# Kernel optimization log

Measured on AMD Instinct MI355X. Metric: run time of the kernel, lower is better.

The kernel has to match this reference:

```python
import jax, jax.numpy as jnp
import numpy as np

def setup_inputs() -> dict:
    key = jax.random.key(0)
    k1, k2, k3, k4 = jax.random.split(key, 4)
    B, T, C, D = 4, 4096, 1024, 128
    x = jax.random.normal(k1, (B, T, C), dtype=jnp.float32)
    Wq = jax.random.normal(k2, (C, D), dtype=jnp.float32) * (C ** -0.5)
    Wk = jax.random.normal(k3, (C, D), dtype=jnp.float32) * (C ** -0.5)
    Wv = jax.random.normal(k4, (C, D), dtype=jnp.float32) * (C ** -0.5)
    return {"x": x, "Wq": Wq, "Wk": Wk, "Wv": Wv}

def reference(x, Wq, Wk, Wv):
    # x: [B,T,C]; Wq/Wk/Wv: [C,D] (nn.Linear bias=False => x @ W)
    B, T, C = x.shape
    q = jnp.einsum('btc,cd->btd', x, Wq)  # [B,T,D]
    k = jnp.einsum('btc,cd->btd', x, Wk)
    v = jnp.einsum('btc,cd->btd', x, Wv)
    dk = q.shape[-1]
    scale = dk ** -0.5
    w = jnp.einsum('btd,bsd->bts', q, k) * scale  # [B,T,T]
    causal = jnp.tril(jnp.ones((T, T), dtype=bool))
    w = jnp.where(causal, w, -jnp.inf)
    w = jax.nn.softmax(w, axis=-1)
    # dropout p=0.0 => identity
    attention = jnp.einsum('bts,bsd->btd', w, v)  # [B,T,D]
    return attention
```

## Files before the change

kernel.cpp:

```cpp
#include <hip/hip_runtime.h>
#include <stdint.h>

typedef __bf16 bf16_t;
typedef bf16_t bf16x8 __attribute__((ext_vector_type(8)));
typedef float f32x4 __attribute__((ext_vector_type(4)));
typedef unsigned short us8 __attribute__((ext_vector_type(8)));
typedef unsigned short us4 __attribute__((ext_vector_type(4)));
typedef unsigned int u32x4 __attribute__((ext_vector_type(4)));

#define B_ 4
#define T_ 4096
#define C_ 1024
#define D_ 128

#define NCHUNK_PB 288
#define QSCALE 0.12751744f

__device__ __forceinline__ uint16_t f2bf(float f) {
    union { float f; uint32_t u; } v; v.f = f;
    uint32_t u = v.u;
    uint32_t r = (u + 0x7fffu + ((u >> 16) & 1u)) >> 16;
    return (uint16_t)r;
}

__device__ __forceinline__ uint16_t bfru(float f) {
    return (uint16_t)((__float_as_uint(f) + 0x8000u) >> 16);
}

__global__ __launch_bounds__(256) void prep_w(const float* __restrict__ Wq,
                                              const float* __restrict__ Wk,
                                              const float* __restrict__ Wv,
                                              uint16_t* __restrict__ WT) {
    int idx = blockIdx.x * 256 + threadIdx.x;
    if (idx >= 3 * D_ * C_) return;
    int w   = idx / (D_ * C_);
    int rem = idx - w * (D_ * C_);
    int n   = rem / C_;
    int k   = rem - n * C_;
    const float* W = (w == 0) ? Wq : (w == 1) ? Wk : Wv;
    WT[idx] = f2bf(W[(size_t)k * D_ + n]);
}

#define GST 72

__global__ __launch_bounds__(256) void qkv_gemm(const float* __restrict__ x,
                                                const uint16_t* __restrict__ WT,
                                                uint16_t* __restrict__ qb,
                                                uint16_t* __restrict__ kb,
                                                uint16_t* __restrict__ vT) {
    __shared__ __align__(16) uint16_t A_lds[64 * GST];
    __shared__ __align__(16) uint16_t W_lds[128 * GST];

    int tid  = threadIdx.x;
    int lane = tid & 63;
    int wave = tid >> 6;
    int quad = lane >> 4;
    int lx   = lane & 15;
    int wm   = wave >> 1, wn = wave & 1;

    int bx   = blockIdx.x;
    int wsel = bx % 3;
    int m0   = (bx / 3) * 64;
    const uint16_t* Wp = WT + (size_t)wsel * (D_ * C_);

    f32x4 acc[2][4];
    for (int mf = 0; mf < 2; mf++)
        for (int nf = 0; nf < 4; nf++)
            acc[mf][nf] = (f32x4){0.f, 0.f, 0.f, 0.f};

    int arow = tid >> 2, acb = (tid & 3) * 16;
    int wrow = tid >> 1, wcb = (tid & 1) * 32;

    for (int k0 = 0; k0 < C_; k0 += 64) {
        {
            const float* xp = x + (size_t)(m0 + arow) * C_ + k0 + acb;
            uint32_t d[8];
#pragma unroll
            for (int j = 0; j < 4; j++) {
                float4 f = *(const float4*)(xp + j * 4);
                uint32_t u0 = __float_as_uint(f.x) + 0x8000u;
                uint32_t u1 = __float_as_uint(f.y) + 0x8000u;
                uint32_t u2 = __float_as_uint(f.z) + 0x8000u;
                uint32_t u3 = __float_as_uint(f.w) + 0x8000u;
                d[2 * j]     = __builtin_amdgcn_perm(u1, u0, 0x07060302);
                d[2 * j + 1] = __builtin_amdgcn_perm(u3, u2, 0x07060302);
            }
            *(u32x4*)&A_lds[arow * GST + acb]     = (u32x4){d[0], d[1], d[2], d[3]};
            *(u32x4*)&A_lds[arow * GST + acb + 8] = (u32x4){d[4], d[5], d[6], d[7]};
        }
        {
            const uint16_t* wp = Wp + (size_t)wrow * C_ + k0 + wcb;
#pragma unroll
            for (int i = 0; i < 4; i++)
                *(us8*)&W_lds[wrow * GST + wcb + i * 8] = *(const us8*)(wp + i * 8);
        }
        __syncthreads();

#pragma unroll
        for (int kc = 0; kc < 2; kc++) {
            bf16x8 af[2];
#pragma unroll
            for (int mf = 0; mf < 2; mf++)
                af[mf] = *(const bf16x8*)&A_lds[(wm * 32 + mf * 16 + lx) * GST + kc * 32 + quad * 8];
#pragma unroll
            for (int nf = 0; nf < 4; nf++) {
                bf16x8 bf = *(const bf16x8*)&W_lds[(wn * 64 + nf * 16 + lx) * GST + kc * 32 + quad * 8];
                acc[0][nf] = __builtin_amdgcn_mfma_f32_16x16x32_bf16(af[0], bf, acc[0][nf], 0, 0, 0);
                acc[1][nf] = __builtin_amdgcn_mfma_f32_16x16x32_bf16(af[1], bf, acc[1][nf], 0, 0, 0);
            }
        }
        __syncthreads();
    }

    int mrow0 = m0 + wm * 32 + quad * 4;
    if (wsel == 2) {
#pragma unroll
        for (int mf = 0; mf < 2; mf++) {
            int mbase = mrow0 + mf * 16;
            int batch = mbase >> 12;
            int t     = mbase & 4095;
#pragma unroll
            for (int nf = 0; nf < 4; nf++) {
                int n = wn * 64 + nf * 16 + lx;
                us4 pv;
#pragma unroll
                for (int r = 0; r < 4; r++) pv[r] = bfru(acc[mf][nf][r]);
                *(us4*)&vT[(size_t)batch * D_ * T_ + (size_t)n * T_ + t] = pv;
            }
        }
    } else {
        uint16_t* dst = (wsel == 0) ? qb : kb;
        float sc = (wsel == 0) ? QSCALE : 1.0f;
#pragma unroll
        for (int mf = 0; mf < 2; mf++)
#pragma unroll
            for (int nf = 0; nf < 4; nf++) {
                int n = wn * 64 + nf * 16 + lx;
#pragma unroll
                for (int r = 0; r < 4; r++)
                    dst[(size_t)(mrow0 + mf * 16 + r) * D_ + n] = bfru(acc[mf][nf][r] * sc);
            }
    }
}

#define KST 136
#define VST 72

__global__ __launch_bounds__(256) void attn(const uint16_t* __restrict__ qb,
                                            const uint16_t* __restrict__ kb,
                                            const uint16_t* __restrict__ vT,
                                            float* __restrict__ part,
                                            float* __restrict__ ml) {
    __shared__ __align__(16) uint16_t K_lds[64 * KST];
    __shared__ __align__(16) uint16_t V_lds[144 * VST];
    __shared__ __align__(16) uint16_t P_lds[4][16 * VST];

    int tid  = threadIdx.x;
    int lane = tid & 63;
    int wave = tid >> 6;
    int quad = lane >> 4;
    int lx   = lane & 15;

    int batch = blockIdx.x & 3;
    int L     = NCHUNK_PB - 1 - (blockIdx.x >> 2);
    int g = 0;
    while (g < 7 && 4 * (g + 1) * (g + 2) <= L) g++;
    int rem   = L - 4 * g * (g + 1);
    int jt    = 8 * g + rem / (g + 1);
    int chunk = rem - (rem / (g + 1)) * (g + 1);
    int lidx  = batch * NCHUNK_PB + L;

    int q0     = jt * 64;
    int st0    = chunk * 8;
    int ntiles = min(8, jt - st0 + 1);

    for (int i = tid; i < 16 * VST; i += 256) {
        int r = i / VST;
        V_lds[(128 + r) * VST + (i - r * VST)] = (r == 0) ? 0x3F80 : 0;
    }

    bf16x8 qf[4];
    {
        const uint16_t* qp = qb + (size_t)(batch * T_ + q0 + wave * 16 + lx) * D_ + quad * 8;
#pragma unroll
        for (int kc = 0; kc < 4; kc++) qf[kc] = *(const bf16x8*)(qp + kc * 32);
    }

    f32x4 o[9];
    for (int i = 0; i < 9; i++) o[i] = (f32x4){0.f, 0.f, 0.f, 0.f};
    float m_i[4];
    for (int r = 0; r < 4; r++) m_i[r] = -INFINITY;

    int krow = tid >> 2, kcb = (tid & 3) * 32;
    int vd   = tid >> 1, vsb = (tid & 1) * 32;

    for (int it = 0; it < ntiles; it++) {
        int s0 = (st0 + it) * 64;
        {
            const uint16_t* kp = kb + (size_t)(batch * T_ + s0 + krow) * D_ + kcb;
#pragma unroll
            for (int i = 0; i < 4; i++)
                *(us8*)&K_lds[krow * KST + kcb + i * 8] = *(const us8*)(kp + i * 8);
        }
        {
            const uint16_t* vp = vT + (size_t)batch * D_ * T_ + (size_t)vd * T_ + s0 + vsb;
#pragma unroll
            for (int i = 0; i < 4; i++)
                *(us8*)&V_lds[vd * VST + vsb + i * 8] = *(const us8*)(vp + i * 8);
        }
        __syncthreads();

        f32x4 s[4];
        for (int nf = 0; nf < 4; nf++) s[nf] = (f32x4){0.f, 0.f, 0.f, 0.f};
#pragma unroll
        for (int kc = 0; kc < 4; kc++)
#pragma unroll
            for (int nf = 0; nf < 4; nf++) {
                bf16x8 kf = *(const bf16x8*)&K_lds[(nf * 16 + lx) * KST + kc * 32 + quad * 8];
                s[nf] = __builtin_amdgcn_mfma_f32_16x16x32_bf16(qf[kc], kf, s[nf], 0, 0, 0);
            }

        float p[4][4];
#pragma unroll
        for (int nf = 0; nf < 4; nf++)
#pragma unroll
            for (int r = 0; r < 4; r++) p[nf][r] = s[nf][r];

        if (st0 + it == jt) {
            int rowg = q0 + wave * 16 + quad * 4;
#pragma unroll
            for (int nf = 0; nf < 4; nf++) {
                int colg = s0 + nf * 16 + lx;
#pragma unroll
                for (int r = 0; r < 4; r++)
                    if (colg > rowg + r) p[nf][r] = -INFINITY;
            }
        }

        float rm[4];
#pragma unroll
        for (int r = 0; r < 4; r++)
            rm[r] = fmaxf(fmaxf(p[0][r], p[1][r]), fmaxf(p[2][r], p[3][r]));
#pragma unroll
        for (int off = 1; off < 16; off <<= 1)
#pragma unroll
            for (int r = 0; r < 4; r++)
                rm[r] = fmaxf(rm[r], __shfl_xor(rm[r], off, 64));

        float alpha[4];
#pragma unroll
        for (int r = 0; r < 4; r++) {
            float mn = fmaxf(m_i[r], rm[r]);
            alpha[r] = exp2f(m_i[r] - mn);
            m_i[r]   = mn;
#pragma unroll
            for (int nf = 0; nf < 4; nf++)
                p[nf][r] = exp2f(p[nf][r] - mn);
        }
#pragma unroll
        for (int i = 0; i < 9; i++)
#pragma unroll
            for (int r = 0; r < 4; r++) o[i][r] *= alpha[r];

#pragma unroll
        for (int nf = 0; nf < 4; nf++)
#pragma unroll
            for (int r = 0; r < 4; r++) {
                uint32_t u  = __float_as_uint(p[nf][r]) + 0x8000u;
                uint32_t pu = (uint32_t)__shfl_xor((int)u, 1, 64);
                uint32_t pk = __builtin_amdgcn_perm(pu, u, 0x07060302);
                if ((lane & 1) == 0)
                    *(uint32_t*)&P_lds[wave][(quad * 4 + r) * VST + nf * 16 + lx] = pk;
            }

        bf16x8 pf[2];
        pf[0] = *(const bf16x8*)&P_lds[wave][lx * VST + quad * 8];
        pf[1] = *(const bf16x8*)&P_lds[wave][lx * VST + 32 + quad * 8];
#pragma unroll
        for (int nf = 0; nf < 9; nf++)
#pragma unroll
            for (int kc = 0; kc < 2; kc++) {
                bf16x8 vf = *(const bf16x8*)&V_lds[(nf * 16 + lx) * VST + kc * 32 + quad * 8];
                o[nf] = __builtin_amdgcn_mfma_f32_16x16x32_bf16(pf[kc], vf, o[nf], 0, 0, 0);
            }
        __syncthreads();
    }

    float* pp = part + (size_t)lidx * (64 * 128);
#pragma unroll
    for (int nf = 0; nf < 8; nf++)
#pragma unroll
        for (int r = 0; r < 4; r++) {
            int lrow = wave * 16 + quad * 4 + r;
            pp[lrow * 128 + nf * 16 + lx] = o[nf][r];
        }
    if (lx == 0) {
#pragma unroll
        for (int r = 0; r < 4; r++) {
            int lrow = wave * 16 + quad * 4 + r;
            ml[(size_t)lidx * 128 + lrow * 2]     = m_i[r];
            ml[(size_t)lidx * 128 + lrow * 2 + 1] = o[8][r];
        }
    }
}

__global__ __launch_bounds__(256) void combine(const float* __restrict__ part,
                                               const float* __restrict__ ml,
                                               float* __restrict__ out) {
    int bidx  = blockIdx.x;
    int batch = bidx >> 6;
    int jt    = bidx & 63;
    int g     = jt >> 3;
    int base  = batch * NCHUNK_PB + jt + g * (jt - 4 * g - 4);
    int nch   = g + 1;

    int tid  = threadIdx.x;
    int lrow = tid >> 2;
    int c0   = (tid & 3) * 32;

    float M = -INFINITY;
    for (int c = 0; c < nch; c++)
        M = fmaxf(M, ml[(size_t)(base + c) * 128 + lrow * 2]);

    float Lsum = 0.f;
    f32x4 acc[8];
#pragma unroll
    for (int i = 0; i < 8; i++) acc[i] = (f32x4){0.f, 0.f, 0.f, 0.f};

    for (int c = 0; c < nch; c++) {
        float m = ml[(size_t)(base + c) * 128 + lrow * 2];
        float l = ml[(size_t)(base + c) * 128 + lrow * 2 + 1];
        float w = exp2f(m - M);
        Lsum += l * w;
        const float* p = part + (size_t)(base + c) * (64 * 128) + lrow * 128 + c0;
#pragma unroll
        for (int i = 0; i < 8; i++) {
            f32x4 v = *(const f32x4*)(p + i * 4);
            acc[i] += v * w;
        }
    }
    float inv = 1.f / Lsum;
    size_t row = (size_t)(batch * T_ + jt * 64 + lrow);
#pragma unroll
    for (int i = 0; i < 8; i++)
        *(f32x4*)(out + row * 128 + c0 + i * 4) = acc[i] * inv;
}

extern "C" void kernel_launch(void* const* d_in, const int* in_sizes, int n_in,
                              void* d_out, int out_size, void* d_ws, size_t ws_size,
                              hipStream_t stream) {
    const float* x  = (const float*)d_in[0];
    const float* Wq = (const float*)d_in[1];
    const float* Wk = (const float*)d_in[2];
    const float* Wv = (const float*)d_in[3];
    float* out = (float*)d_out;

    uint16_t* ws = (uint16_t*)d_ws;
    uint16_t* qb = ws;
    uint16_t* kb = qb + (size_t)16384 * 128;
    uint16_t* vT = kb + (size_t)16384 * 128;
    uint16_t* WT = vT + (size_t)16384 * 128;
    float* part = (float*)(WT + (size_t)3 * D_ * C_);
    float* ml   = part + (size_t)4 * NCHUNK_PB * 64 * 128;

    prep_w<<<dim3((3 * D_ * C_ + 255) / 256), dim3(256), 0, stream>>>(Wq, Wk, Wv, WT);
    qkv_gemm<<<dim3(3 * (16384 / 64)), dim3(256), 0, stream>>>(x, WT, qb, kb, vT);
    attn<<<dim3(B_ * NCHUNK_PB), dim3(256), 0, stream>>>(qb, kb, vT, part, ml);
    combine<<<dim3(B_ * (T_ / 64)), dim3(256), 0, stream>>>(part, ml, out);
}
```

Before: 210.8 us.

## Register-prefetch next tiles in GEMM and attention; store partials as bf16

Both the QKV GEMM and the attention kernel now load the next K/V (or x/W) tile from global memory into registers while MFMAs run on the current LDS tile. The barrier placement is rearranged so that one sync before the LDS write replaces the trailing sync. Attention partial outputs are written as bf16 instead of fp32, which halves partial-buffer traffic in attn and combine. The cost is higher register pressure and some loss of precision in the unnormalized partial sums.

```diff
diff --git a/kernel.cpp b/kernel.cpp
--- a/kernel.cpp
+++ b/kernel.cpp
@@ -25,6 +25,10 @@
 
 __device__ __forceinline__ uint16_t bfru(float f) {
     return (uint16_t)((__float_as_uint(f) + 0x8000u) >> 16);
+}
+
+__device__ __forceinline__ float bf2f(uint16_t u) {
+    return __uint_as_float((uint32_t)u << 16);
 }
 
 __global__ __launch_bounds__(256) void prep_w(const float* __restrict__ Wq,
@@ -71,30 +75,40 @@
     int arow = tid >> 2, acb = (tid & 3) * 16;
     int wrow = tid >> 1, wcb = (tid & 1) * 32;
 
+    float4 xr[4];
+    us8    wr[4];
+    auto ldG = [&](int k0) {
+        const float* xp = x + (size_t)(m0 + arow) * C_ + k0 + acb;
+#pragma unroll
+        for (int j = 0; j < 4; j++) xr[j] = *(const float4*)(xp + j * 4);
+        const uint16_t* wp = Wp + (size_t)wrow * C_ + k0 + wcb;
+#pragma unroll
+        for (int i = 0; i < 4; i++) wr[i] = *(const us8*)(wp + i * 8);
+    };
+
+    ldG(0);
     for (int k0 = 0; k0 < C_; k0 += 64) {
+        __syncthreads();
         {
-            const float* xp = x + (size_t)(m0 + arow) * C_ + k0 + acb;
             uint32_t d[8];
 #pragma unroll
             for (int j = 0; j < 4; j++) {
-                float4 f = *(const float4*)(xp + j * 4);
-                uint32_t u0 = __float_as_uint(f.x) + 0x8000u;
-                uint32_t u1 = __float_as_uint(f.y) + 0x8000u;
-                uint32_t u2 = __float_as_uint(f.z) + 0x8000u;
-                uint32_t u3 = __float_as_uint(f.w) + 0x8000u;
+                uint32_t u0 = __float_as_uint(xr[j].x) + 0x8000u;
+                uint32_t u1 = __float_as_uint(xr[j].y) + 0x8000u;
+                uint32_t u2 = __float_as_uint(xr[j].z) + 0x8000u;
+                uint32_t u3 = __float_as_uint(xr[j].w) + 0x8000u;
                 d[2 * j]     = __builtin_amdgcn_perm(u1, u0, 0x07060302);
                 d[2 * j + 1] = __builtin_amdgcn_perm(u3, u2, 0x07060302);
             }
             *(u32x4*)&A_lds[arow * GST + acb]     = (u32x4){d[0], d[1], d[2], d[3]};
             *(u32x4*)&A_lds[arow * GST + acb + 8] = (u32x4){d[4], d[5], d[6], d[7]};
         }
-        {
-            const uint16_t* wp = Wp + (size_t)wrow * C_ + k0 + wcb;
-#pragma unroll
-            for (int i = 0; i < 4; i++)
-                *(us8*)&W_lds[wrow * GST + wcb + i * 8] = *(const us8*)(wp + i * 8);
-        }
+#pragma unroll
+        for (int i = 0; i < 4; i++)
+            *(us8*)&W_lds[wrow * GST + wcb + i * 8] = wr[i];
         __syncthreads();
+
+        if (k0 + 64 < C_) ldG(k0 + 64);
 
 #pragma unroll
         for (int kc = 0; kc < 2; kc++) {
@@ -109,7 +123,6 @@
                 acc[1][nf] = __builtin_amdgcn_mfma_f32_16x16x32_bf16(af[1], bf, acc[1][nf], 0, 0, 0);
             }
         }
-        __syncthreads();
     }
 
     int mrow0 = m0 + wm * 32 + quad * 4;
@@ -149,7 +162,7 @@
 __global__ __launch_bounds__(256) void attn(const uint16_t* __restrict__ qb,
                                             const uint16_t* __restrict__ kb,
                                             const uint16_t* __restrict__ vT,
-                                            float* __restrict__ part,
+                                            uint16_t* __restrict__ part,
                                             float* __restrict__ ml) {
     __shared__ __align__(16) uint16_t K_lds[64 * KST];
     __shared__ __align__(16) uint16_t V_lds[144 * VST];
@@ -194,21 +207,30 @@
     int krow = tid >> 2, kcb = (tid & 3) * 32;
     int vd   = tid >> 1, vsb = (tid & 1) * 32;
 
+    us8 kreg[4], vreg[4];
+    auto ldG = [&](int st) {
+        const uint16_t* kp = kb + (size_t)(batch * T_ + st * 64 + krow) * D_ + kcb;
+#pragma unroll
+        for (int i = 0; i < 4; i++) kreg[i] = *(const us8*)(kp + i * 8);
+        const uint16_t* vp = vT + (size_t)batch * D_ * T_ + (size_t)vd * T_ + st * 64 + vsb;
+#pragma unroll
+        for (int i = 0; i < 4; i++) vreg[i] = *(const us8*)(vp + i * 8);
+    };
+
+    ldG(st0);
     for (int it = 0; it < ntiles; it++) {
+        __syncthreads();
+#pragma unroll
+        for (int i = 0; i < 4; i++)
+            *(us8*)&K_lds[krow * KST + kcb + i * 8] = kreg[i];
+#pragma unroll
+        for (int i = 0; i < 4; i++)
+            *(us8*)&V_lds[vd * VST + vsb + i * 8] = vreg[i];
+        __syncthreads();
+
+        if (it + 1 < ntiles) ldG(st0 + it + 1);
+
         int s0 = (st0 + it) * 64;
-        {
-            const uint16_t* kp = kb + (size_t)(batch * T_ + s0 + krow) * D_ + kcb;
-#pragma unroll
-            for (int i = 0; i < 4; i++)
-                *(us8*)&K_lds[krow * KST + kcb + i * 8] = *(const us8*)(kp + i * 8);
-        }
-        {
-            const uint16_t* vp = vT + (size_t)batch * D_ * T_ + (size_t)vd * T_ + s0 + vsb;
-#pragma unroll
-            for (int i = 0; i < 4; i++)
-                *(us8*)&V_lds[vd * VST + vsb + i * 8] = *(const us8*)(vp + i * 8);
-        }
-        __syncthreads();
 
         f32x4 s[4];
         for (int nf = 0; nf < 4; nf++) s[nf] = (f32x4){0.f, 0.f, 0.f, 0.f};
@@ -283,16 +305,15 @@
                 bf16x8 vf = *(const bf16x8*)&V_lds[(nf * 16 + lx) * VST + kc * 32 + quad * 8];
                 o[nf] = __builtin_amdgcn_mfma_f32_16x16x32_bf16(pf[kc], vf, o[nf], 0, 0, 0);
             }
-        __syncthreads();
-    }
-
-    float* pp = part + (size_t)lidx * (64 * 128);
+    }
+
+    uint16_t* pp = part + (size_t)lidx * (64 * 128);
 #pragma unroll
     for (int nf = 0; nf < 8; nf++)
 #pragma unroll
         for (int r = 0; r < 4; r++) {
             int lrow = wave * 16 + quad * 4 + r;
-            pp[lrow * 128 + nf * 16 + lx] = o[nf][r];
+            pp[lrow * 128 + nf * 16 + lx] = bfru(o[nf][r]);
         }
     if (lx == 0) {
 #pragma unroll
@@ -304,7 +325,7 @@
     }
 }
 
-__global__ __launch_bounds__(256) void combine(const float* __restrict__ part,
+__global__ __launch_bounds__(256) void combine(const uint16_t* __restrict__ part,
                                                const float* __restrict__ ml,
                                                float* __restrict__ out) {
     int bidx  = blockIdx.x;
@@ -332,11 +353,13 @@
         float l = ml[(size_t)(base + c) * 128 + lrow * 2 + 1];
         float w = exp2f(m - M);
         Lsum += l * w;
-        const float* p = part + (size_t)(base + c) * (64 * 128) + lrow * 128 + c0;
-#pragma unroll
-        for (int i = 0; i < 8; i++) {
-            f32x4 v = *(const f32x4*)(p + i * 4);
-            acc[i] += v * w;
+        const uint16_t* p = part + (size_t)(base + c) * (64 * 128) + lrow * 128 + c0;
+#pragma unroll
+        for (int i = 0; i < 4; i++) {
+            us8 v = *(const us8*)(p + i * 8);
+#pragma unroll
+            for (int j = 0; j < 8; j++)
+                acc[i * 2 + (j >> 2)][j & 3] += bf2f(v[j]) * w;
         }
     }
     float inv = 1.f / Lsum;
@@ -360,8 +383,8 @@
     uint16_t* kb = qb + (size_t)16384 * 128;
     uint16_t* vT = kb + (size_t)16384 * 128;
     uint16_t* WT = vT + (size_t)16384 * 128;
-    float* part = (float*)(WT + (size_t)3 * D_ * C_);
-    float* ml   = part + (size_t)4 * NCHUNK_PB * 64 * 128;
+    uint16_t* part = WT + (size_t)3 * D_ * C_;
+    float* ml = (float*)(part + (size_t)4 * NCHUNK_PB * 64 * 128);
 
     prep_w<<<dim3((3 * D_ * C_ + 255) / 256), dim3(256), 0, stream>>>(Wq, Wk, Wv, WT);
     qkv_gemm<<<dim3(3 * (16384 / 64)), dim3(256), 0, stream>>>(x, WT, qb, kb, vT);
```

Measured after the change: 214.9 us. About the same (+2.0%).

## Use 128-row query tiles with 8 waves, bf16 partials, explicit row sums

Applied to the files above, without the earlier changes.

Each attention block now covers 128 query rows with 512 threads (8 waves), so every K/V tile loaded into LDS is reused by twice as many rows, and the number of chunks per batch is halved. The row-sum trick that used an extra ones-column of V is replaced by an explicit shuffle reduction of the exp values. Waves whose rows lie entirely above the tile skip the MFMA work. Partial outputs are stored as bf16, halving partial-buffer traffic in the combine step at some cost in precision.

```diff
diff --git a/kernel.cpp b/kernel.cpp
--- a/kernel.cpp
+++ b/kernel.cpp
@@ -13,7 +13,7 @@
 #define C_ 1024
 #define D_ 128
 
-#define NCHUNK_PB 288
+#define NCHUNK_PB 144
 #define QSCALE 0.12751744f
 
 __device__ __forceinline__ uint16_t f2bf(float f) {
@@ -25,6 +25,10 @@
 
 __device__ __forceinline__ uint16_t bfru(float f) {
     return (uint16_t)((__float_as_uint(f) + 0x8000u) >> 16);
+}
+
+__device__ __forceinline__ float bf2f(uint16_t u) {
+    return __uint_as_float((uint32_t)u << 16);
 }
 
 __global__ __launch_bounds__(256) void prep_w(const float* __restrict__ Wq,
@@ -146,14 +150,14 @@
 #define KST 136
 #define VST 72
 
-__global__ __launch_bounds__(256) void attn(const uint16_t* __restrict__ qb,
-                                            const uint16_t* __restrict__ kb,
-                                            const uint16_t* __restrict__ vT,
-                                            float* __restrict__ part,
-                                            float* __restrict__ ml) {
+__global__ __launch_bounds__(512, 6) void attn(const uint16_t* __restrict__ qb,
+                                               const uint16_t* __restrict__ kb,
+                                               const uint16_t* __restrict__ vT,
+                                               uint16_t* __restrict__ part,
+                                               float* __restrict__ ml) {
     __shared__ __align__(16) uint16_t K_lds[64 * KST];
-    __shared__ __align__(16) uint16_t V_lds[144 * VST];
-    __shared__ __align__(16) uint16_t P_lds[4][16 * VST];
+    __shared__ __align__(16) uint16_t V_lds[128 * VST];
+    __shared__ __align__(16) uint16_t P_lds[8][16 * VST];
 
     int tid  = threadIdx.x;
     int lane = tid & 63;
@@ -164,155 +168,163 @@
     int batch = blockIdx.x & 3;
     int L     = NCHUNK_PB - 1 - (blockIdx.x >> 2);
     int g = 0;
-    while (g < 7 && 4 * (g + 1) * (g + 2) <= L) g++;
-    int rem   = L - 4 * g * (g + 1);
-    int jt    = 8 * g + rem / (g + 1);
+    while (g < 7 && 2 * (g + 1) * (g + 2) <= L) g++;
+    int rem   = L - 2 * g * (g + 1);
+    int jt2   = 4 * g + rem / (g + 1);
     int chunk = rem - (rem / (g + 1)) * (g + 1);
     int lidx  = batch * NCHUNK_PB + L;
 
-    int q0     = jt * 64;
+    int q0     = jt2 * 128;
     int st0    = chunk * 8;
-    int ntiles = min(8, jt - st0 + 1);
-
-    for (int i = tid; i < 16 * VST; i += 256) {
-        int r = i / VST;
-        V_lds[(128 + r) * VST + (i - r * VST)] = (r == 0) ? 0x3F80 : 0;
-    }
+    int ntiles = min(8, 2 * jt2 + 2 - st0);
+    int wrow0  = q0 + wave * 16;
 
     bf16x8 qf[4];
     {
-        const uint16_t* qp = qb + (size_t)(batch * T_ + q0 + wave * 16 + lx) * D_ + quad * 8;
+        const uint16_t* qp = qb + (size_t)(batch * T_ + wrow0 + lx) * D_ + quad * 8;
 #pragma unroll
         for (int kc = 0; kc < 4; kc++) qf[kc] = *(const bf16x8*)(qp + kc * 32);
     }
 
-    f32x4 o[9];
-    for (int i = 0; i < 9; i++) o[i] = (f32x4){0.f, 0.f, 0.f, 0.f};
-    float m_i[4];
-    for (int r = 0; r < 4; r++) m_i[r] = -INFINITY;
-
-    int krow = tid >> 2, kcb = (tid & 3) * 32;
-    int vd   = tid >> 1, vsb = (tid & 1) * 32;
+    f32x4 o[8];
+    for (int i = 0; i < 8; i++) o[i] = (f32x4){0.f, 0.f, 0.f, 0.f};
+    float m_i[4], l_i[4];
+    for (int r = 0; r < 4; r++) { m_i[r] = -INFINITY; l_i[r] = 0.f; }
+
+    int krow = tid >> 3, kcb = (tid & 7) * 16;
+    int vd   = tid >> 2, vsb = (tid & 3) * 16;
 
     for (int it = 0; it < ntiles; it++) {
         int s0 = (st0 + it) * 64;
         {
             const uint16_t* kp = kb + (size_t)(batch * T_ + s0 + krow) * D_ + kcb;
-#pragma unroll
-            for (int i = 0; i < 4; i++)
-                *(us8*)&K_lds[krow * KST + kcb + i * 8] = *(const us8*)(kp + i * 8);
+            *(us8*)&K_lds[krow * KST + kcb]     = *(const us8*)kp;
+            *(us8*)&K_lds[krow * KST + kcb + 8] = *(const us8*)(kp + 8);
         }
         {
             const uint16_t* vp = vT + (size_t)batch * D_ * T_ + (size_t)vd * T_ + s0 + vsb;
-#pragma unroll
-            for (int i = 0; i < 4; i++)
-                *(us8*)&V_lds[vd * VST + vsb + i * 8] = *(const us8*)(vp + i * 8);
+            *(us8*)&V_lds[vd * VST + vsb]     = *(const us8*)vp;
+            *(us8*)&V_lds[vd * VST + vsb + 8] = *(const us8*)(vp + 8);
         }
         __syncthreads();
 
-        f32x4 s[4];
-        for (int nf = 0; nf < 4; nf++) s[nf] = (f32x4){0.f, 0.f, 0.f, 0.f};
-#pragma unroll
-        for (int kc = 0; kc < 4; kc++)
-#pragma unroll
-            for (int nf = 0; nf < 4; nf++) {
-                bf16x8 kf = *(const bf16x8*)&K_lds[(nf * 16 + lx) * KST + kc * 32 + quad * 8];
-                s[nf] = __builtin_amdgcn_mfma_f32_16x16x32_bf16(qf[kc], kf, s[nf], 0, 0, 0);
-            }
-
-        float p[4][4];
-#pragma unroll
-        for (int nf = 0; nf < 4; nf++)
-#pragma unroll
-            for (int r = 0; r < 4; r++) p[nf][r] = s[nf][r];
-
-        if (st0 + it == jt) {
-            int rowg = q0 + wave * 16 + quad * 4;
-#pragma unroll
-            for (int nf = 0; nf < 4; nf++) {
-                int colg = s0 + nf * 16 + lx;
+        if (s0 <= wrow0 + 15) {
+            f32x4 s[4];
+            for (int nf = 0; nf < 4; nf++) s[nf] = (f32x4){0.f, 0.f, 0.f, 0.f};
+#pragma unroll
+            for (int kc = 0; kc < 4; kc++)
+#pragma unroll
+                for (int nf = 0; nf < 4; nf++) {
+                    bf16x8 kf = *(const bf16x8*)&K_lds[(nf * 16 + lx) * KST + kc * 32 + quad * 8];
+                    s[nf] = __builtin_amdgcn_mfma_f32_16x16x32_bf16(qf[kc], kf, s[nf], 0, 0, 0);
+                }
+
+            float p[4][4];
+#pragma unroll
+            for (int nf = 0; nf < 4; nf++)
+#pragma unroll
+                for (int r = 0; r < 4; r++) p[nf][r] = s[nf][r];
+
+            if (s0 + 63 > wrow0) {
+                int rowg = wrow0 + quad * 4;
+#pragma unroll
+                for (int nf = 0; nf < 4; nf++) {
+                    int colg = s0 + nf * 16 + lx;
+#pragma unroll
+                    for (int r = 0; r < 4; r++)
+                        if (colg > rowg + r) p[nf][r] = -INFINITY;
+                }
+            }
+
+            float rm[4];
+#pragma unroll
+            for (int r = 0; r < 4; r++)
+                rm[r] = fmaxf(fmaxf(p[0][r], p[1][r]), fmaxf(p[2][r], p[3][r]));
+#pragma unroll
+            for (int off = 1; off < 16; off <<= 1)
 #pragma unroll
                 for (int r = 0; r < 4; r++)
-                    if (colg > rowg + r) p[nf][r] = -INFINITY;
-            }
-        }
-
-        float rm[4];
-#pragma unroll
-        for (int r = 0; r < 4; r++)
-            rm[r] = fmaxf(fmaxf(p[0][r], p[1][r]), fmaxf(p[2][r], p[3][r]));
-#pragma unroll
-        for (int off = 1; off < 16; off <<= 1)
-#pragma unroll
-            for (int r = 0; r < 4; r++)
-                rm[r] = fmaxf(rm[r], __shfl_xor(rm[r], off, 64));
-
-        float alpha[4];
-#pragma unroll
-        for (int r = 0; r < 4; r++) {
-            float mn = fmaxf(m_i[r], rm[r]);
-            alpha[r] = exp2f(m_i[r] - mn);
-            m_i[r]   = mn;
+                    rm[r] = fmaxf(rm[r], __shfl_xor(rm[r], off, 64));
+
+            float alpha[4], rs[4];
+#pragma unroll
+            for (int r = 0; r < 4; r++) {
+                float mn = fmaxf(m_i[r], rm[r]);
+                alpha[r] = exp2f(m_i[r] - mn);
+                m_i[r]   = mn;
+                float sum = 0.f;
+#pragma unroll
+                for (int nf = 0; nf < 4; nf++) {
+                    float e = exp2f(p[nf][r] - mn);
+                    p[nf][r] = e;
+                    sum += e;
+                }
+                rs[r] = sum;
+            }
+#pragma unroll
+            for (int off = 1; off < 16; off <<= 1)
+#pragma unroll
+                for (int r = 0; r < 4; r++)
+                    rs[r] += __shfl_xor(rs[r], off, 64);
+#pragma unroll
+            for (int r = 0; r < 4; r++) l_i[r] = l_i[r] * alpha[r] + rs[r];
+#pragma unroll
+            for (int i = 0; i < 8; i++)
+#pragma unroll
+                for (int r = 0; r < 4; r++) o[i][r] *= alpha[r];
+
 #pragma unroll
             for (int nf = 0; nf < 4; nf++)
-                p[nf][r] = exp2f(p[nf][r] - mn);
-        }
-#pragma unroll
-        for (int i = 0; i < 9; i++)
-#pragma unroll
-            for (int r = 0; r < 4; r++) o[i][r] *= alpha[r];
-
-#pragma unroll
-        for (int nf = 0; nf < 4; nf++)
-#pragma unroll
-            for (int r = 0; r < 4; r++) {
-                uint32_t u  = __float_as_uint(p[nf][r]) + 0x8000u;
-                uint32_t pu = (uint32_t)__shfl_xor((int)u, 1, 64);
-                uint32_t pk = __builtin_amdgcn_perm(pu, u, 0x07060302);
-                if ((lane & 1) == 0)
-                    *(uint32_t*)&P_lds[wave][(quad * 4 + r) * VST + nf * 16 + lx] = pk;
-            }
-
-        bf16x8 pf[2];
-        pf[0] = *(const bf16x8*)&P_lds[wave][lx * VST + quad * 8];
-        pf[1] = *(const bf16x8*)&P_lds[wave][lx * VST + 32 + quad * 8];
-#pragma unroll
-        for (int nf = 0; nf < 9; nf++)
-#pragma unroll
-            for (int kc = 0; kc < 2; kc++) {
-                bf16x8 vf = *(const bf16x8*)&V_lds[(nf * 16 + lx) * VST + kc * 32 + quad * 8];
-                o[nf] = __builtin_amdgcn_mfma_f32_16x16x32_bf16(pf[kc], vf, o[nf], 0, 0, 0);
-            }
+#pragma unroll
+                for (int r = 0; r < 4; r++) {
+                    uint32_t u  = __float_as_uint(p[nf][r]) + 0x8000u;
+                    uint32_t pu = (uint32_t)__shfl_xor((int)u, 1, 64);
+                    uint32_t pk = __builtin_amdgcn_perm(pu, u, 0x07060302);
+                    if ((lane & 1) == 0)
+                        *(uint32_t*)&P_lds[wave][(quad * 4 + r) * VST + nf * 16 + lx] = pk;
+                }
+
+            bf16x8 pf[2];
+            pf[0] = *(const bf16x8*)&P_lds[wave][lx * VST + quad * 8];
+            pf[1] = *(const bf16x8*)&P_lds[wave][lx * VST + 32 + quad * 8];
+#pragma unroll
+            for (int nf = 0; nf < 8; nf++)
+#pragma unroll
+                for (int kc = 0; kc < 2; kc++) {
+                    bf16x8 vf = *(const bf16x8*)&V_lds[(nf * 16 + lx) * VST + kc * 32 + quad * 8];
+                    o[nf] = __builtin_amdgcn_mfma_f32_16x16x32_bf16(pf[kc], vf, o[nf], 0, 0, 0);
+                }
+        }
         __syncthreads();
     }
 
-    float* pp = part + (size_t)lidx * (64 * 128);
+    uint16_t* pp = part + (size_t)lidx * (128 * 128);
 #pragma unroll
     for (int nf = 0; nf < 8; nf++)
 #pragma unroll
         for (int r = 0; r < 4; r++) {
             int lrow = wave * 16 + quad * 4 + r;
-            pp[lrow * 128 + nf * 16 + lx] = o[nf][r];
+            pp[lrow * 128 + nf * 16 + lx] = bfru(o[nf][r]);
         }
     if (lx == 0) {
 #pragma unroll
         for (int r = 0; r < 4; r++) {
             int lrow = wave * 16 + quad * 4 + r;
-            ml[(size_t)lidx * 128 + lrow * 2]     = m_i[r];
-            ml[(size_t)lidx * 128 + lrow * 2 + 1] = o[8][r];
-        }
-    }
-}
-
-__global__ __launch_bounds__(256) void combine(const float* __restrict__ part,
+            ml[(size_t)lidx * 256 + lrow * 2]     = m_i[r];
+            ml[(size_t)lidx * 256 + lrow * 2 + 1] = l_i[r];
+        }
+    }
+}
+
+__global__ __launch_bounds__(512) void combine(const uint16_t* __restrict__ part,
                                                const float* __restrict__ ml,
                                                float* __restrict__ out) {
     int bidx  = blockIdx.x;
-    int batch = bidx >> 6;
-    int jt    = bidx & 63;
-    int g     = jt >> 3;
-    int base  = batch * NCHUNK_PB + jt + g * (jt - 4 * g - 4);
-    int nch   = g + 1;
+    int batch = bidx >> 5;
+    int jt2   = bidx & 31;
+    int q     = jt2 >> 2, r = jt2 & 3;
+    int base  = batch * NCHUNK_PB + 2 * q * (q + 1) + r * (q + 1);
+    int nch   = q + 1;
 
     int tid  = threadIdx.x;
     int lrow = tid >> 2;
@@ -320,7 +332,7 @@
 
     float M = -INFINITY;
     for (int c = 0; c < nch; c++)
-        M = fmaxf(M, ml[(size_t)(base + c) * 128 + lrow * 2]);
+        M = fmaxf(M, ml[(size_t)(base + c) * 256 + lrow * 2]);
 
     float Lsum = 0.f;
     f32x4 acc[8];
@@ -328,19 +340,21 @@
     for (int i = 0; i < 8; i++) acc[i] = (f32x4){0.f, 0.f, 0.f, 0.f};
 
     for (int c = 0; c < nch; c++) {
-        float m = ml[(size_t)(base + c) * 128 + lrow * 2];
-        float l = ml[(size_t)(base + c) * 128 + lrow * 2 + 1];
+        float m = ml[(size_t)(base + c) * 256 + lrow * 2];
+        float l = ml[(size_t)(base + c) * 256 + lrow * 2 + 1];
         float w = exp2f(m - M);
         Lsum += l * w;
-        const float* p = part + (size_t)(base + c) * (64 * 128) + lrow * 128 + c0;
-#pragma unroll
-        for (int i = 0; i < 8; i++) {
-            f32x4 v = *(const f32x4*)(p + i * 4);
-            acc[i] += v * w;
+        const uint16_t* p = part + (size_t)(base + c) * (128 * 128) + lrow * 128 + c0;
+#pragma unroll
+        for (int i = 0; i < 4; i++) {
+            us8 v = *(const us8*)(p + i * 8);
+#pragma unroll
+            for (int j = 0; j < 8; j++)
+                acc[i * 2 + (j >> 2)][j & 3] += bf2f(v[j]) * w;
         }
     }
     float inv = 1.f / Lsum;
-    size_t row = (size_t)(batch * T_ + jt * 64 + lrow);
+    size_t row = (size_t)(batch * T_ + jt2 * 128 + lrow);
 #pragma unroll
     for (int i = 0; i < 8; i++)
         *(f32x4*)(out + row * 128 + c0 + i * 4) = acc[i] * inv;
@@ -360,11 +374,11 @@
     uint16_t* kb = qb + (size_t)16384 * 128;
     uint16_t* vT = kb + (size_t)16384 * 128;
     uint16_t* WT = vT + (size_t)16384 * 128;
-    float* part = (float*)(WT + (size_t)3 * D_ * C_);
-    float* ml   = part + (size_t)4 * NCHUNK_PB * 64 * 128;
+    uint16_t* part = WT + (size_t)3 * D_ * C_;
+    float* ml = (float*)(part + (size_t)4 * NCHUNK_PB * 128 * 128);
 
     prep_w<<<dim3((3 * D_ * C_ + 255) / 256), dim3(256), 0, stream>>>(Wq, Wk, Wv, WT);
     qkv_gemm<<<dim3(3 * (16384 / 64)), dim3(256), 0, stream>>>(x, WT, qb, kb, vT);
-    attn<<<dim3(B_ * NCHUNK_PB), dim3(256), 0, stream>>>(qb, kb, vT, part, ml);
-    combine<<<dim3(B_ * (T_ / 64)), dim3(256), 0, stream>>>(part, ml, out);
-}
+    attn<<<dim3(B_ * NCHUNK_PB), dim3(512), 0, stream>>>(qb, kb, vT, part, ml);
+    combine<<<dim3(B_ * (T_ / 128)), dim3(512), 0, stream>>>(part, ml, out);
+}
```

Result: slower. 257.9 us (+22.4%).
